# Performance work log

Measured on AMD Instinct MI355X. Metric: run time of the kernel, lower is better.

## Reference

```python
import jax, jax.numpy as jnp
import numpy as np

B, SEQ, DIM, D, K = 32, 2048, 512, 512, 128


def _ln(x, g, b, eps=1e-5):
    m = x.mean(-1, keepdims=True)
    v = ((x - m) ** 2).mean(-1, keepdims=True)
    return (x - m) / jnp.sqrt(v + eps) * g + b


def _gelu(v):
    return jax.nn.gelu(v, approximate=False)


def _diff_topk(s, k, t):
    # s: (B, N) scores; iterative relaxed top-k (Xie & Ermon style).
    def step(carry, _):
        a = jax.nn.softmax(carry / t, axis=-1)
        carry = carry + jnp.log(jnp.clip(1.0 - a, 1e-6, 1.0))
        return carry, a
    _, Ws = jax.lax.scan(step, s, None, length=k)  # (k, B, N)
    return jnp.transpose(Ws, (1, 0, 2))            # (B, k, N)


def setup_inputs():
    key = jax.random.key(0)
    ks = jax.random.split(key, 6)
    w = lambda k_, shape: jax.random.normal(k_, shape, dtype=jnp.float32) * 0.02
    return {
        'x': jax.random.normal(ks[0], (B, SEQ, DIM), dtype=jnp.float32),
        'tau': jnp.array(0.0, dtype=jnp.float32),
        'ln1_g': jnp.ones((DIM,), jnp.float32), 'ln1_b': jnp.zeros((DIM,), jnp.float32),
        'W1': w(ks[1], (DIM, D)), 'b1': jnp.zeros((D,), jnp.float32),
        'ln2_g': jnp.ones((SEQ,), jnp.float32), 'ln2_b': jnp.zeros((SEQ,), jnp.float32),
        'W2': w(ks[2], (SEQ, SEQ)), 'b2': jnp.zeros((SEQ,), jnp.float32),
        'ln3_g': jnp.ones((D,), jnp.float32), 'ln3_b': jnp.zeros((D,), jnp.float32),
        'W3': w(ks[3], (D, D + 1)), 'b3': jnp.zeros((D + 1,), jnp.float32),
        'ln4_g': jnp.ones((D,), jnp.float32), 'ln4_b': jnp.zeros((D,), jnp.float32),
        'W4': w(ks[4], (D, DIM)), 'b4': jnp.zeros((DIM,), jnp.float32),
    }


def reference(x, tau, ln1_g, ln1_b, W1, b1, ln2_g, ln2_b, W2, b2,
              ln3_g, ln3_b, W3, b3, ln4_g, ln4_b, W4, b4):
    # tok_proj: LN(dim) -> Linear(dim, D) -> GELU
    x_tok = _gelu(_ln(x, ln1_g, ln1_b) @ W1 + b1)                  # (B, N, D)
    # ch_proj over the token axis: LN(seq) -> Linear(seq, seq) -> GELU
    xt = jnp.swapaxes(x_tok, 1, 2)                                  # (B, D, N)
    x_ch = jnp.swapaxes(_gelu(_ln(xt, ln2_g, ln2_b) @ W2 + b2), 1, 2)
    # proj -> split score | features
    h = _ln(x_tok + x_ch, ln3_g, ln3_b) @ W3 + b3                   # (B, N, D+1)
    x_score, x_proj = h[..., 0], h[..., 1:]
    t = jax.nn.sigmoid(jnp.clip(tau, -2.0, 5.0))
    Wmat = _diff_topk(x_score, K, t)                                # (B, k, N)
    Z = jnp.einsum('bkn,bnd->bkd', Wmat, x_proj)                    # soft gather
    Y = jnp.einsum('bkn,bkd->bnd', Wmat, Z)                         # soft scatter
    return _ln(x_proj + Y, ln4_g, ln4_b) @ W4 + b4                  # (B, N, dim)
```

## Files before the change

kernel.cpp:

```cpp
#include <hip/hip_runtime.h>
#include <math.h>

#define B_   32
#define SEQ_ 2048
#define DIM_ 512
#define KSEL 128

typedef _Float16 f16;
typedef _Float16 half8 __attribute__((ext_vector_type(8)));
typedef float floatx4 __attribute__((ext_vector_type(4)));

#define LSTRH 40

__device__ __forceinline__ float gelu_exact(float v) {
  return 0.5f * v * (1.0f + erff(v * 0.70710678118654752440f));
}

__global__ __launch_bounds__(256) void rowstats512(const float* __restrict__ X,
                                                   float* __restrict__ mean,
                                                   float* __restrict__ rstd) {
  int row = blockIdx.x * 4 + (threadIdx.x >> 6);
  int l = threadIdx.x & 63;
  const float4* p = (const float4*)(X + (size_t)row * 512);
  float4 v0 = p[l * 2], v1 = p[l * 2 + 1];
  float s = v0.x + v0.y + v0.z + v0.w + v1.x + v1.y + v1.z + v1.w;
  float q = v0.x*v0.x + v0.y*v0.y + v0.z*v0.z + v0.w*v0.w
          + v1.x*v1.x + v1.y*v1.y + v1.z*v1.z + v1.w*v1.w;
#pragma unroll
  for (int off = 32; off > 0; off >>= 1) {
    s += __shfl_down(s, off);
    q += __shfl_down(q, off);
  }
  if (l == 0) {
    float m = s * (1.0f / 512.0f);
    float var = q * (1.0f / 512.0f) - m * m;
    mean[row] = m;
    rstd[row] = rsqrtf(var + 1e-5f);
  }
}

__global__ __launch_bounds__(256) void rowstats512_f16(const f16* __restrict__ X,
                                                       float* __restrict__ mean,
                                                       float* __restrict__ rstd) {
  int row = blockIdx.x * 4 + (threadIdx.x >> 6);
  int l = threadIdx.x & 63;
  half8 h = *(const half8*)(X + (size_t)row * 512 + l * 8);
  float s = 0.f, q = 0.f;
#pragma unroll
  for (int i = 0; i < 8; ++i) { float v = (float)h[i]; s += v; q += v * v; }
#pragma unroll
  for (int off = 32; off > 0; off >>= 1) {
    s += __shfl_down(s, off);
    q += __shfl_down(q, off);
  }
  if (l == 0) {
    float m = s * (1.0f / 512.0f);
    float var = q * (1.0f / 512.0f) - m * m;
    mean[row] = m;
    rstd[row] = rsqrtf(var + 1e-5f);
  }
}

__global__ __launch_bounds__(512) void colstats_part(const f16* __restrict__ xtok,
                                                     float2* __restrict__ part) {
  int b = blockIdx.x >> 3, pr = blockIdx.x & 7;
  int d = threadIdx.x;
  const f16* src = xtok + ((size_t)b * SEQ_ + (size_t)pr * 256) * 512 + d;
  float s = 0.f, q = 0.f;
#pragma unroll 4
  for (int i = 0; i < 256; ++i) {
    float v = (float)src[(size_t)i * 512];
    s += v; q += v * v;
  }
  part[(size_t)blockIdx.x * 512 + d] = make_float2(s, q);
}

__global__ __launch_bounds__(256) void colstats_fin(const float2* __restrict__ part,
                                                    float* __restrict__ mean,
                                                    float* __restrict__ rstd) {
  int idx = blockIdx.x * 256 + threadIdx.x;
  int b = idx >> 9;
  float s = 0.f, q = 0.f;
#pragma unroll
  for (int p = 0; p < 8; ++p) {
    float2 v = part[((size_t)(b * 8 + p)) * 512 + (idx & 511)];
    s += v.x; q += v.y;
  }
  float m = s * (1.0f / 2048.0f);
  mean[idx] = m;
  rstd[idx] = rsqrtf(q * (1.0f / 2048.0f) - m * m + 1e-5f);
}

template <typename T>
__global__ __launch_bounds__(256) void transpose_cvt(const T* __restrict__ src,
                                                     f16* __restrict__ dst,
                                                     int R, int C, long sb, long db) {
  __shared__ float tile[32][33];
  const T* s = src + (long)blockIdx.z * sb;
  f16* d = dst + (long)blockIdx.z * db;
  int c0 = blockIdx.x * 32, r0 = blockIdx.y * 32;
  int tx = threadIdx.x, ty = threadIdx.y;
#pragma unroll
  for (int i = 0; i < 4; ++i) {
    int r = r0 + ty + i * 8, c = c0 + tx;
    if (r < R && c < C) tile[ty + i * 8][tx] = (float)s[(long)r * C + c];
  }
  __syncthreads();
#pragma unroll
  for (int i = 0; i < 4; ++i) {
    int c = c0 + ty + i * 8, r = r0 + tx;
    if (c < C && r < R) d[(long)c * R + r] = (f16)tile[tx][ty + i * 8];
  }
}

__global__ __launch_bounds__(256) void trans2_kernel(const f16* __restrict__ xtok,
    const float* __restrict__ mean2, const float* __restrict__ rstd2,
    const float* __restrict__ g2, const float* __restrict__ bl2,
    f16* __restrict__ A2) {
  __shared__ float tile[32][33];
  int b = blockIdx.z;
  const f16* src = xtok + (long)b * SEQ_ * 512;
  f16* dst = A2 + (long)b * 512 * SEQ_;
  int d0 = blockIdx.x * 32, s0 = blockIdx.y * 32;
  int tx = threadIdx.x, ty = threadIdx.y;
  float m = mean2[b * 512 + d0 + tx];
  float rs = rstd2[b * 512 + d0 + tx];
#pragma unroll
  for (int i = 0; i < 4; ++i) {
    int s = s0 + ty + i * 8;
    float v = (float)src[(long)s * 512 + d0 + tx];
    tile[ty + i * 8][tx] = (v - m) * rs * g2[s] + bl2[s];
  }
  __syncthreads();
#pragma unroll
  for (int i = 0; i < 4; ++i) {
    int d = d0 + ty + i * 8, s = s0 + tx;
    dst[(long)d * SEQ_ + s] = (f16)tile[tx][ty + i * 8];
  }
}


__device__ __forceinline__ void stage_f16(const f16* __restrict__ src, long ld,
                                          int row0, int k0, f16* S, int t) {
  int row = t >> 1, kc = (t & 1) * 16;
  const f16* p = src + (long)(row0 + row) * ld + k0 + kc;
  half8 v0 = *(const half8*)(p);
  half8 v1 = *(const half8*)(p + 8);
  *(half8*)(S + row * LSTRH + kc) = v0;
  *(half8*)(S + row * LSTRH + kc + 8) = v1;
}

__device__ __forceinline__ void stage_a_f32(const float* __restrict__ src, long ld,
                                            int row0, int k0, f16* S, int t) {
  int row = t >> 1, kc = (t & 1) * 16;
  const float* p = src + (long)(row0 + row) * ld + k0 + kc;
  float v[16];
#pragma unroll
  for (int i = 0; i < 4; ++i) {
    float4 q = ((const float4*)p)[i];
    v[i * 4 + 0] = q.x; v[i * 4 + 1] = q.y; v[i * 4 + 2] = q.z; v[i * 4 + 3] = q.w;
  }
  half8 o0, o1;
#pragma unroll
  for (int i = 0; i < 8; ++i) { o0[i] = (f16)v[i]; o1[i] = (f16)v[i + 8]; }
  *(half8*)(S + row * LSTRH + kc) = o0;
  *(half8*)(S + row * LSTRH + kc + 8) = o1;
}

__device__ __forceinline__ void stage_a_ln_f32(const float* __restrict__ src, long ld,
    const float* __restrict__ mean, const float* __restrict__ rstd,
    const float* __restrict__ g, const float* __restrict__ bl,
    int row0, int k0, f16* S, int t) {
  int row = t >> 1, kc = (t & 1) * 16;
  int r = row0 + row, c = k0 + kc;
  float m = mean[r], sd = rstd[r];
  const float* p = src + (long)r * ld + c;
  float v[16], gv[16], bv[16];
#pragma unroll
  for (int i = 0; i < 4; ++i) {
    float4 q = ((const float4*)p)[i];
    v[i*4+0]=q.x; v[i*4+1]=q.y; v[i*4+2]=q.z; v[i*4+3]=q.w;
    float4 gq = ((const float4*)(g + c))[i];
    gv[i*4+0]=gq.x; gv[i*4+1]=gq.y; gv[i*4+2]=gq.z; gv[i*4+3]=gq.w;
    float4 bq = ((const float4*)(bl + c))[i];
    bv[i*4+0]=bq.x; bv[i*4+1]=bq.y; bv[i*4+2]=bq.z; bv[i*4+3]=bq.w;
  }
  half8 o0, o1;
#pragma unroll
  for (int i = 0; i < 8; ++i) {
    o0[i] = (f16)((v[i] - m) * sd * gv[i] + bv[i]);
    o1[i] = (f16)((v[i + 8] - m) * sd * gv[i + 8] + bv[i + 8]);
  }
  *(half8*)(S + row * LSTRH + kc) = o0;
  *(half8*)(S + row * LSTRH + kc + 8) = o1;
}

__device__ __forceinline__ void stage_a_ln_f16(const f16* __restrict__ src, long ld,
    const float* __restrict__ mean, const float* __restrict__ rstd,
    const float* __restrict__ g, const float* __restrict__ bl,
    int row0, int k0, f16* S, int t) {
  int row = t >> 1, kc = (t & 1) * 16;
  int r = row0 + row, c = k0 + kc;
  float m = mean[r], sd = rstd[r];
  const f16* p = src + (long)r * ld + c;
  half8 h0 = *(const half8*)(p);
  half8 h1 = *(const half8*)(p + 8);
  float gv[16], bv[16];
#pragma unroll
  for (int i = 0; i < 4; ++i) {
    float4 gq = ((const float4*)(g + c))[i];
    gv[i*4+0]=gq.x; gv[i*4+1]=gq.y; gv[i*4+2]=gq.z; gv[i*4+3]=gq.w;
    float4 bq = ((const float4*)(bl + c))[i];
    bv[i*4+0]=bq.x; bv[i*4+1]=bq.y; bv[i*4+2]=bq.z; bv[i*4+3]=bq.w;
  }
  half8 o0, o1;
#pragma unroll
  for (int i = 0; i < 8; ++i) {
    o0[i] = (f16)(((float)h0[i] - m) * sd * gv[i] + bv[i]);
    o1[i] = (f16)(((float)h1[i] - m) * sd * gv[i + 8] + bv[i + 8]);
  }
  *(half8*)(S + row * LSTRH + kc) = o0;
  *(half8*)(S + row * LSTRH + kc + 8) = o1;
}

__device__ __forceinline__ void mfma_step(const f16* As, const f16* Bs, int lane,
                                          int wr, int wc, floatx4 acc[4][4]) {
  int kc = (lane >> 4) * 8;
  int rl = lane & 15;
  half8 a[4], b[4];
#pragma unroll
  for (int mi = 0; mi < 4; ++mi)
    a[mi] = *(const half8*)(As + (wr * 64 + mi * 16 + rl) * LSTRH + kc);
#pragma unroll
  for (int ni = 0; ni < 4; ++ni)
    b[ni] = *(const half8*)(Bs + (wc * 64 + ni * 16 + rl) * LSTRH + kc);
#pragma unroll
  for (int mi = 0; mi < 4; ++mi)
#pragma unroll
    for (int ni = 0; ni < 4; ++ni)
      acc[mi][ni] = __builtin_amdgcn_mfma_f32_16x16x32_f16(a[mi], b[ni], acc[mi][ni], 0, 0, 0);
}

#define GEMM_PROLOG \
  __shared__ f16 As[128 * LSTRH]; \
  __shared__ f16 Bs[128 * LSTRH]; \
  int t = threadIdx.x; \
  int lane = t & 63, w = t >> 6, wr = w >> 1, wc = w & 1; \
  floatx4 acc[4][4]; \
  _Pragma("unroll") for (int mi = 0; mi < 4; ++mi) \
  _Pragma("unroll") for (int ni = 0; ni < 4; ++ni) acc[mi][ni] = (floatx4){0.f,0.f,0.f,0.f};

__global__ __launch_bounds__(256) void g1_kernel(const float* __restrict__ x,
    const float* __restrict__ mean, const float* __restrict__ rstd,
    const float* __restrict__ g1, const float* __restrict__ bl1,
    const f16* __restrict__ W1T, const float* __restrict__ b1,
    f16* __restrict__ xtok) {
  GEMM_PROLOG
  int m0 = blockIdx.y * 128, n0 = blockIdx.x * 128;
  for (int k0 = 0; k0 < 512; k0 += 32) {
    stage_a_ln_f32(x, 512, mean, rstd, g1, bl1, m0, k0, As, t);
    stage_f16(W1T, 512, n0, k0, Bs, t);
    __syncthreads();
    mfma_step(As, Bs, lane, wr, wc, acc);
    __syncthreads();
  }
#pragma unroll
  for (int mi = 0; mi < 4; ++mi)
#pragma unroll
    for (int ni = 0; ni < 4; ++ni) {
      int c = n0 + wc * 64 + ni * 16 + (lane & 15);
      float bias = b1[c];
      int r0 = m0 + wr * 64 + mi * 16 + (lane >> 4) * 4;
#pragma unroll
      for (int j = 0; j < 4; ++j)
        xtok[(long)(r0 + j) * 512 + c] = (f16)gelu_exact(acc[mi][ni][j] + bias);
    }
}

__global__ __launch_bounds__(256) void g2_kernel(const f16* __restrict__ W2T,
    const f16* __restrict__ A2, const float* __restrict__ b2,
    const f16* __restrict__ xtok, f16* __restrict__ xsum) {
  GEMM_PROLOG
  int b = blockIdx.z;
  int m0 = blockIdx.y * 128, n0 = blockIdx.x * 128;
  const f16* A2b = A2 + (long)b * 512 * SEQ_;
  const f16* xtb = xtok + (long)b * SEQ_ * 512;
  f16* xsb = xsum + (long)b * SEQ_ * 512;
  for (int k0 = 0; k0 < SEQ_; k0 += 32) {
    stage_f16(W2T, SEQ_, m0, k0, As, t);
    stage_f16(A2b, SEQ_, n0, k0, Bs, t);
    __syncthreads();
    mfma_step(As, Bs, lane, wr, wc, acc);
    __syncthreads();
  }
#pragma unroll
  for (int mi = 0; mi < 4; ++mi)
#pragma unroll
    for (int ni = 0; ni < 4; ++ni) {
      int c = n0 + wc * 64 + ni * 16 + (lane & 15);
      int r0 = m0 + wr * 64 + mi * 16 + (lane >> 4) * 4;
#pragma unroll
      for (int j = 0; j < 4; ++j) {
        int r = r0 + j;
        long idx = (long)r * 512 + c;
        float v = gelu_exact(acc[mi][ni][j] + b2[r]);
        xsb[idx] = (f16)((float)xtb[idx] + v);
      }
    }
}

__global__ __launch_bounds__(256) void g3_kernel(const f16* __restrict__ xsum,
    const float* __restrict__ mean, const float* __restrict__ rstd,
    const float* __restrict__ g3, const float* __restrict__ bl3,
    const f16* __restrict__ BT , const float* __restrict__ b3,
    f16* __restrict__ xproj) {
  GEMM_PROLOG
  int m0 = blockIdx.y * 128, n0 = blockIdx.x * 128;
  for (int k0 = 0; k0 < 512; k0 += 32) {
    stage_a_ln_f16(xsum, 512, mean, rstd, g3, bl3, m0, k0, As, t);
    stage_f16(BT, 512, n0, k0, Bs, t);
    __syncthreads();
    mfma_step(As, Bs, lane, wr, wc, acc);
    __syncthreads();
  }
#pragma unroll
  for (int mi = 0; mi < 4; ++mi)
#pragma unroll
    for (int ni = 0; ni < 4; ++ni) {
      int c = n0 + wc * 64 + ni * 16 + (lane & 15);
      float bias = b3[c + 1];
      int r0 = m0 + wr * 64 + mi * 16 + (lane >> 4) * 4;
#pragma unroll
      for (int j = 0; j < 4; ++j)
        xproj[(long)(r0 + j) * 512 + c] = (f16)(acc[mi][ni][j] + bias);
    }
}

__global__ __launch_bounds__(256) void score_kernel(const f16* __restrict__ xsum,
    const float* __restrict__ mean, const float* __restrict__ rstd,
    const float* __restrict__ g3, const float* __restrict__ bl3,
    const f16* __restrict__ w3c , const float* __restrict__ b3,
    float* __restrict__ xscore) {
  int row = blockIdx.x * 4 + (threadIdx.x >> 6);
  int l = threadIdx.x & 63;
  float m = mean[row], sd = rstd[row];
  half8 h = *(const half8*)(xsum + (long)row * 512 + l * 8);
  half8 wv = *(const half8*)(w3c + l * 8);
  float acc = 0.f;
#pragma unroll
  for (int i = 0; i < 8; ++i) {
    int d = l * 8 + i;
    float v = ((float)h[i] - m) * sd * g3[d] + bl3[d];
    acc += v * (float)wv[i];
  }
#pragma unroll
  for (int off = 32; off > 0; off >>= 1) acc += __shfl_down(acc, off);
  if (l == 0) xscore[row] = acc + b3[0];
}

__global__ __launch_bounds__(256) void topk_kernel(const float* __restrict__ xscore,
                                                   const float* __restrict__ tau,
                                                   float* __restrict__ Wm) {
  int b = blockIdx.x, t = threadIdx.x;
  __shared__ float red[4];
  float tv = fminf(fmaxf(tau[0], -2.0f), 5.0f);
  float temp = 1.0f / (1.0f + expf(-tv));
  float it = 1.0f / temp;
  float c[8];
  const float* xs = xscore + (size_t)b * SEQ_;
#pragma unroll
  for (int i = 0; i < 8; ++i) c[i] = xs[t * 8 + i];
  for (int k = 0; k < KSEL; ++k) {
    float e[8];
    float p = 0.f;
#pragma unroll
    for (int i = 0; i < 8; ++i) { e[i] = expf(c[i] * it); p += e[i]; }
#pragma unroll
    for (int off = 32; off > 0; off >>= 1) p += __shfl_down(p, off);
    if ((t & 63) == 0) red[t >> 6] = p;
    __syncthreads();
    float S = red[0] + red[1] + red[2] + red[3];
    float iS = 1.0f / S;
    float a[8];
#pragma unroll
    for (int i = 0; i < 8; ++i) a[i] = e[i] * iS;
    float* dst = Wm + ((size_t)b * KSEL + k) * SEQ_ + t * 8;
    *(float4*)(dst) = make_float4(a[0], a[1], a[2], a[3]);
    *(float4*)(dst + 4) = make_float4(a[4], a[5], a[6], a[7]);
#pragma unroll
    for (int i = 0; i < 8; ++i) c[i] += logf(fmaxf(1.0f - a[i], 1e-6f));
    __syncthreads();
  }
}

__global__ __launch_bounds__(256) void gz_kernel(const float* __restrict__ Wm,
    const f16* __restrict__ xprojT, float* __restrict__ Z) {
  GEMM_PROLOG
  int b = blockIdx.z;
  int n0 = blockIdx.x * 128;
  const float* A = Wm + (long)b * KSEL * SEQ_;
  const f16* BT = xprojT + (long)b * 512 * SEQ_;
  float* Zb = Z + (long)b * KSEL * 512;
  for (int k0 = 0; k0 < SEQ_; k0 += 32) {
    stage_a_f32(A, SEQ_, 0, k0, As, t);
    stage_f16(BT, SEQ_, n0, k0, Bs, t);
    __syncthreads();
    mfma_step(As, Bs, lane, wr, wc, acc);
    __syncthreads();
  }
#pragma unroll
  for (int mi = 0; mi < 4; ++mi)
#pragma unroll
    for (int ni = 0; ni < 4; ++ni) {
      int c = n0 + wc * 64 + ni * 16 + (lane & 15);
      int r0 = wr * 64 + mi * 16 + (lane >> 4) * 4;
#pragma unroll
      for (int j = 0; j < 4; ++j)
        Zb[(long)(r0 + j) * 512 + c] = acc[mi][ni][j];
    }
}

__global__ __launch_bounds__(256) void gy_kernel(const f16* __restrict__ WmT,
    const f16* __restrict__ ZT, const f16* __restrict__ xproj,
    f16* __restrict__ rbuf) {
  GEMM_PROLOG
  int b = blockIdx.z;
  int m0 = blockIdx.y * 128, n0 = blockIdx.x * 128;
  const f16* A = WmT + (long)b * SEQ_ * KSEL;
  const f16* BT = ZT + (long)b * 512 * KSEL;
  const f16* xpb = xproj + (long)b * SEQ_ * 512;
  f16* rb = rbuf + (long)b * SEQ_ * 512;
  for (int k0 = 0; k0 < KSEL; k0 += 32) {
    stage_f16(A, KSEL, m0, k0, As, t);
    stage_f16(BT, KSEL, n0, k0, Bs, t);
    __syncthreads();
    mfma_step(As, Bs, lane, wr, wc, acc);
    __syncthreads();
  }
#pragma unroll
  for (int mi = 0; mi < 4; ++mi)
#pragma unroll
    for (int ni = 0; ni < 4; ++ni) {
      int c = n0 + wc * 64 + ni * 16 + (lane & 15);
      int r0 = m0 + wr * 64 + mi * 16 + (lane >> 4) * 4;
#pragma unroll
      for (int j = 0; j < 4; ++j) {
        long idx = (long)(r0 + j) * 512 + c;
        rb[idx] = (f16)((float)xpb[idx] + acc[mi][ni][j]);
      }
    }
}

__global__ __launch_bounds__(256) void g4_kernel(const f16* __restrict__ rbuf,
    const float* __restrict__ mean, const float* __restrict__ rstd,
    const float* __restrict__ g4, const float* __restrict__ bl4,
    const f16* __restrict__ W4T, const float* __restrict__ b4,
    float* __restrict__ out) {
  GEMM_PROLOG
  int m0 = blockIdx.y * 128, n0 = blockIdx.x * 128;
  for (int k0 = 0; k0 < 512; k0 += 32) {
    stage_a_ln_f16(rbuf, 512, mean, rstd, g4, bl4, m0, k0, As, t);
    stage_f16(W4T, 512, n0, k0, Bs, t);
    __syncthreads();
    mfma_step(As, Bs, lane, wr, wc, acc);
    __syncthreads();
  }
#pragma unroll
  for (int mi = 0; mi < 4; ++mi)
#pragma unroll
    for (int ni = 0; ni < 4; ++ni) {
      int c = n0 + wc * 64 + ni * 16 + (lane & 15);
      float bias = b4[c];
      int r0 = m0 + wr * 64 + mi * 16 + (lane >> 4) * 4;
#pragma unroll
      for (int j = 0; j < 4; ++j)
        out[(long)(r0 + j) * 512 + c] = acc[mi][ni][j] + bias;
    }
}

extern "C" void kernel_launch(void* const* d_in, const int* in_sizes, int n_in,
                              void* d_out, int out_size, void* d_ws, size_t ws_size,
                              hipStream_t stream) {
  const float* x    = (const float*)d_in[0];
  const float* tau  = (const float*)d_in[1];
  const float* g1   = (const float*)d_in[2];
  const float* bl1  = (const float*)d_in[3];
  const float* W1   = (const float*)d_in[4];
  const float* b1   = (const float*)d_in[5];
  const float* g2   = (const float*)d_in[6];
  const float* bl2  = (const float*)d_in[7];
  const float* W2   = (const float*)d_in[8];
  const float* b2   = (const float*)d_in[9];
  const float* g3   = (const float*)d_in[10];
  const float* bl3  = (const float*)d_in[11];
  const float* W3   = (const float*)d_in[12];
  const float* b3   = (const float*)d_in[13];
  const float* g4   = (const float*)d_in[14];
  const float* bl4  = (const float*)d_in[15];
  const float* W4   = (const float*)d_in[16];
  const float* b4   = (const float*)d_in[17];
  float* out = (float*)d_out;

  const long NTOK = (long)B_ * SEQ_;

  char* ws = (char*)d_ws;
  f16* regA   = (f16*)(ws);
  f16* regB   = (f16*)(ws + (64l << 20));
  float* Z    = (float*)(ws + (128l << 20));
  f16* ZT     = (f16*)(ws + (136l << 20));
  f16* WmT    = (f16*)(ws + (140l << 20));
  f16* W1T    = (f16*)(ws + (156l << 20));
  f16* W2T    = (f16*)(ws + (157l << 20));
  f16* W3T    = (f16*)(ws + (165l << 20));
  f16* W4T    = (f16*)(ws + (166l << 20));
  float* xscore = (float*)(ws + (167l << 20));
  float* meanA  = (float*)(ws + (168l << 20));
  float* rstdA  = meanA + NTOK;
  float* mean2  = rstdA + NTOK;
  float* rstd2  = mean2 + B_ * 512;
  float2* part  = (float2*)(rstd2 + B_ * 512);

  f16* xtok   = (f16*)d_out;
  float* Wm   = (float*)((char*)d_out + (64l << 20));
  f16* xprojT = (f16*)d_out;

  f16* A2    = regA;
  f16* xsum  = regB;
  f16* xproj = regA;
  f16* rbuf  = regB;

  dim3 tb(32, 8);

  transpose_cvt<float><<<dim3(16, 16, 1), tb, 0, stream>>>(W1, W1T, 512, 512, 0, 0);
  transpose_cvt<float><<<dim3(64, 64, 1), tb, 0, stream>>>(W2, W2T, 2048, 2048, 0, 0);
  transpose_cvt<float><<<dim3(17, 16, 1), tb, 0, stream>>>(W3, W3T, 512, 513, 0, 0);
  transpose_cvt<float><<<dim3(16, 16, 1), tb, 0, stream>>>(W4, W4T, 512, 512, 0, 0);

  rowstats512<<<NTOK / 4, 256, 0, stream>>>(x, meanA, rstdA);
  g1_kernel<<<dim3(4, 512), 256, 0, stream>>>(x, meanA, rstdA, g1, bl1, W1T, b1, xtok);

  colstats_part<<<B_ * 8, 512, 0, stream>>>(xtok, part);
  colstats_fin<<<64, 256, 0, stream>>>(part, mean2, rstd2);
  trans2_kernel<<<dim3(16, 64, B_), tb, 0, stream>>>(xtok, mean2, rstd2, g2, bl2, A2);
  g2_kernel<<<dim3(4, 16, B_), 256, 0, stream>>>(W2T, A2, b2, xtok, xsum);

  rowstats512_f16<<<NTOK / 4, 256, 0, stream>>>(xsum, meanA, rstdA);
  score_kernel<<<NTOK / 4, 256, 0, stream>>>(xsum, meanA, rstdA, g3, bl3, W3T, b3, xscore);
  g3_kernel<<<dim3(4, 512), 256, 0, stream>>>(xsum, meanA, rstdA, g3, bl3, W3T + 512, b3, xproj);

  topk_kernel<<<B_, 256, 0, stream>>>(xscore, tau, Wm);

  transpose_cvt<f16><<<dim3(16, 64, B_), tb, 0, stream>>>(xproj, xprojT, 2048, 512,
      (long)SEQ_ * 512, (long)512 * SEQ_);
  transpose_cvt<float><<<dim3(64, 4, B_), tb, 0, stream>>>(Wm, WmT, 128, 2048,
      (long)KSEL * SEQ_, (long)SEQ_ * KSEL);

  gz_kernel<<<dim3(4, 1, B_), 256, 0, stream>>>(Wm, xprojT, Z);
  transpose_cvt<float><<<dim3(16, 4, B_), tb, 0, stream>>>(Z, ZT, 128, 512,
      (long)KSEL * 512, (long)512 * KSEL);

  gy_kernel<<<dim3(4, 16, B_), 256, 0, stream>>>(WmT, ZT, xproj, rbuf);

  rowstats512_f16<<<NTOK / 4, 256, 0, stream>>>(rbuf, meanA, rstdA);
  g4_kernel<<<dim3(4, 512), 256, 0, stream>>>(rbuf, meanA, rstdA, g4, bl4, W4T, b4, out);
}
```

Baseline: 980.8 us.

## Stage f16 GEMM tiles via global_load_lds and split-K the gather GEMM

```diff
diff --git a/kernel.cpp b/kernel.cpp
--- a/kernel.cpp
+++ b/kernel.cpp
@@ -10,7 +10,7 @@
 typedef _Float16 half8 __attribute__((ext_vector_type(8)));
 typedef float floatx4 __attribute__((ext_vector_type(4)));
 
-#define LSTRH 40
+#define LSTR2 32
 
 __device__ __forceinline__ float gelu_exact(float v) {
   return 0.5f * v * (1.0f + erff(v * 0.70710678118654752440f));
@@ -140,31 +140,19 @@
 }
 
 
-__device__ __forceinline__ void stage_f16(const f16* __restrict__ src, long ld,
+__device__ __forceinline__ void stage_gll(const f16* __restrict__ src, long ld,
                                           int row0, int k0, f16* S, int t) {
-  int row = t >> 1, kc = (t & 1) * 16;
-  const f16* p = src + (long)(row0 + row) * ld + k0 + kc;
-  half8 v0 = *(const half8*)(p);
-  half8 v1 = *(const half8*)(p + 8);
-  *(half8*)(S + row * LSTRH + kc) = v0;
-  *(half8*)(S + row * LSTRH + kc + 8) = v1;
-}
-
-__device__ __forceinline__ void stage_a_f32(const float* __restrict__ src, long ld,
-                                            int row0, int k0, f16* S, int t) {
-  int row = t >> 1, kc = (t & 1) * 16;
-  const float* p = src + (long)(row0 + row) * ld + k0 + kc;
-  float v[16];
-#pragma unroll
-  for (int i = 0; i < 4; ++i) {
-    float4 q = ((const float4*)p)[i];
-    v[i * 4 + 0] = q.x; v[i * 4 + 1] = q.y; v[i * 4 + 2] = q.z; v[i * 4 + 3] = q.w;
-  }
-  half8 o0, o1;
-#pragma unroll
-  for (int i = 0; i < 8; ++i) { o0[i] = (f16)v[i]; o1[i] = (f16)v[i + 8]; }
-  *(half8*)(S + row * LSTRH + kc) = o0;
-  *(half8*)(S + row * LSTRH + kc + 8) = o1;
+  int w = t >> 6, lane = t & 63;
+  int r = lane >> 2, c8 = (lane & 3) * 8;
+#pragma unroll
+  for (int i = 0; i < 2; ++i) {
+    int chunk = w * 2 + i;
+    const f16* g = src + (long)(row0 + chunk * 16 + r) * ld + k0 + c8;
+    f16* l = S + chunk * 16 * LSTR2;
+    __builtin_amdgcn_global_load_lds(
+        (const __attribute__((address_space(1))) void*)g,
+        (__attribute__((address_space(3))) void*)l, 16, 0, 0);
+  }
 }
 
 __device__ __forceinline__ void stage_a_ln_f32(const float* __restrict__ src, long ld,
@@ -191,8 +179,8 @@
     o0[i] = (f16)((v[i] - m) * sd * gv[i] + bv[i]);
     o1[i] = (f16)((v[i + 8] - m) * sd * gv[i + 8] + bv[i + 8]);
   }
-  *(half8*)(S + row * LSTRH + kc) = o0;
-  *(half8*)(S + row * LSTRH + kc + 8) = o1;
+  *(half8*)(S + row * LSTR2 + kc) = o0;
+  *(half8*)(S + row * LSTR2 + kc + 8) = o1;
 }
 
 __device__ __forceinline__ void stage_a_ln_f16(const f16* __restrict__ src, long ld,
@@ -219,8 +207,8 @@
     o0[i] = (f16)(((float)h0[i] - m) * sd * gv[i] + bv[i]);
     o1[i] = (f16)(((float)h1[i] - m) * sd * gv[i + 8] + bv[i + 8]);
   }
-  *(half8*)(S + row * LSTRH + kc) = o0;
-  *(half8*)(S + row * LSTRH + kc + 8) = o1;
+  *(half8*)(S + row * LSTR2 + kc) = o0;
+  *(half8*)(S + row * LSTR2 + kc + 8) = o1;
 }
 
 __device__ __forceinline__ void mfma_step(const f16* As, const f16* Bs, int lane,
@@ -230,10 +218,10 @@
   half8 a[4], b[4];
 #pragma unroll
   for (int mi = 0; mi < 4; ++mi)
-    a[mi] = *(const half8*)(As + (wr * 64 + mi * 16 + rl) * LSTRH + kc);
+    a[mi] = *(const half8*)(As + (wr * 64 + mi * 16 + rl) * LSTR2 + kc);
 #pragma unroll
   for (int ni = 0; ni < 4; ++ni)
-    b[ni] = *(const half8*)(Bs + (wc * 64 + ni * 16 + rl) * LSTRH + kc);
+    b[ni] = *(const half8*)(Bs + (wc * 64 + ni * 16 + rl) * LSTR2 + kc);
 #pragma unroll
   for (int mi = 0; mi < 4; ++mi)
 #pragma unroll
@@ -242,8 +230,8 @@
 }
 
 #define GEMM_PROLOG \
-  __shared__ f16 As[128 * LSTRH]; \
-  __shared__ f16 Bs[128 * LSTRH]; \
+  __shared__ __attribute__((aligned(16))) f16 As[128 * LSTR2]; \
+  __shared__ __attribute__((aligned(16))) f16 Bs[128 * LSTR2]; \
   int t = threadIdx.x; \
   int lane = t & 63, w = t >> 6, wr = w >> 1, wc = w & 1; \
   floatx4 acc[4][4]; \
@@ -259,7 +247,7 @@
   int m0 = blockIdx.y * 128, n0 = blockIdx.x * 128;
   for (int k0 = 0; k0 < 512; k0 += 32) {
     stage_a_ln_f32(x, 512, mean, rstd, g1, bl1, m0, k0, As, t);
-    stage_f16(W1T, 512, n0, k0, Bs, t);
+    stage_gll(W1T, 512, n0, k0, Bs, t);
     __syncthreads();
     mfma_step(As, Bs, lane, wr, wc, acc);
     __syncthreads();
@@ -287,8 +275,8 @@
   const f16* xtb = xtok + (long)b * SEQ_ * 512;
   f16* xsb = xsum + (long)b * SEQ_ * 512;
   for (int k0 = 0; k0 < SEQ_; k0 += 32) {
-    stage_f16(W2T, SEQ_, m0, k0, As, t);
-    stage_f16(A2b, SEQ_, n0, k0, Bs, t);
+    stage_gll(W2T, SEQ_, m0, k0, As, t);
+    stage_gll(A2b, SEQ_, n0, k0, Bs, t);
     __syncthreads();
     mfma_step(As, Bs, lane, wr, wc, acc);
     __syncthreads();
@@ -318,7 +306,7 @@
   int m0 = blockIdx.y * 128, n0 = blockIdx.x * 128;
   for (int k0 = 0; k0 < 512; k0 += 32) {
     stage_a_ln_f16(xsum, 512, mean, rstd, g3, bl3, m0, k0, As, t);
-    stage_f16(BT, 512, n0, k0, Bs, t);
+    stage_gll(BT, 512, n0, k0, Bs, t);
     __syncthreads();
     mfma_step(As, Bs, lane, wr, wc, acc);
     __syncthreads();
@@ -360,7 +348,7 @@
 
 __global__ __launch_bounds__(256) void topk_kernel(const float* __restrict__ xscore,
                                                    const float* __restrict__ tau,
-                                                   float* __restrict__ Wm) {
+                                                   f16* __restrict__ Wm) {
   int b = blockIdx.x, t = threadIdx.x;
   __shared__ float red[4];
   float tv = fminf(fmaxf(tau[0], -2.0f), 5.0f);
@@ -382,28 +370,28 @@
     float S = red[0] + red[1] + red[2] + red[3];
     float iS = 1.0f / S;
     float a[8];
-#pragma unroll
-    for (int i = 0; i < 8; ++i) a[i] = e[i] * iS;
-    float* dst = Wm + ((size_t)b * KSEL + k) * SEQ_ + t * 8;
-    *(float4*)(dst) = make_float4(a[0], a[1], a[2], a[3]);
-    *(float4*)(dst + 4) = make_float4(a[4], a[5], a[6], a[7]);
+    half8 h;
+#pragma unroll
+    for (int i = 0; i < 8; ++i) { a[i] = e[i] * iS; h[i] = (f16)a[i]; }
+    *(half8*)(Wm + ((size_t)b * KSEL + k) * SEQ_ + t * 8) = h;
 #pragma unroll
     for (int i = 0; i < 8; ++i) c[i] += logf(fmaxf(1.0f - a[i], 1e-6f));
     __syncthreads();
   }
 }
 
-__global__ __launch_bounds__(256) void gz_kernel(const float* __restrict__ Wm,
-    const f16* __restrict__ xprojT, float* __restrict__ Z) {
+__global__ __launch_bounds__(256) void gz_kernel(const f16* __restrict__ Wm,
+    const f16* __restrict__ xprojT, float* __restrict__ Zpart) {
   GEMM_PROLOG
-  int b = blockIdx.z;
+  int b = blockIdx.z, kc = blockIdx.y;
   int n0 = blockIdx.x * 128;
-  const float* A = Wm + (long)b * KSEL * SEQ_;
+  const f16* A = Wm + (long)b * KSEL * SEQ_;
   const f16* BT = xprojT + (long)b * 512 * SEQ_;
-  float* Zb = Z + (long)b * KSEL * 512;
-  for (int k0 = 0; k0 < SEQ_; k0 += 32) {
-    stage_a_f32(A, SEQ_, 0, k0, As, t);
-    stage_f16(BT, SEQ_, n0, k0, Bs, t);
+  float* Zb = Zpart + ((long)b * 2 + kc) * KSEL * 512;
+  int kbeg = kc * 1024, kend = kbeg + 1024;
+  for (int k0 = kbeg; k0 < kend; k0 += 32) {
+    stage_gll(A, SEQ_, 0, k0, As, t);
+    stage_gll(BT, SEQ_, n0, k0, Bs, t);
     __syncthreads();
     mfma_step(As, Bs, lane, wr, wc, acc);
     __syncthreads();
@@ -418,6 +406,28 @@
       for (int j = 0; j < 4; ++j)
         Zb[(long)(r0 + j) * 512 + c] = acc[mi][ni][j];
     }
+}
+
+__global__ __launch_bounds__(256) void ztrans_kernel(const float* __restrict__ Zpart,
+                                                     f16* __restrict__ ZT) {
+  __shared__ float tile[32][33];
+  int b = blockIdx.z;
+  int c0 = blockIdx.x * 32, r0 = blockIdx.y * 32;
+  int tx = threadIdx.x, ty = threadIdx.y;
+  const float* p0 = Zpart + ((long)b * 2 + 0) * KSEL * 512;
+  const float* p1 = Zpart + ((long)b * 2 + 1) * KSEL * 512;
+#pragma unroll
+  for (int i = 0; i < 4; ++i) {
+    int r = r0 + ty + i * 8, c = c0 + tx;
+    tile[ty + i * 8][tx] = p0[(long)r * 512 + c] + p1[(long)r * 512 + c];
+  }
+  __syncthreads();
+  f16* d = ZT + (long)b * 512 * KSEL;
+#pragma unroll
+  for (int i = 0; i < 4; ++i) {
+    int c = c0 + ty + i * 8, r = r0 + tx;
+    d[(long)c * KSEL + r] = (f16)tile[tx][ty + i * 8];
+  }
 }
 
 __global__ __launch_bounds__(256) void gy_kernel(const f16* __restrict__ WmT,
@@ -431,8 +441,8 @@
   const f16* xpb = xproj + (long)b * SEQ_ * 512;
   f16* rb = rbuf + (long)b * SEQ_ * 512;
   for (int k0 = 0; k0 < KSEL; k0 += 32) {
-    stage_f16(A, KSEL, m0, k0, As, t);
-    stage_f16(BT, KSEL, n0, k0, Bs, t);
+    stage_gll(A, KSEL, m0, k0, As, t);
+    stage_gll(BT, KSEL, n0, k0, Bs, t);
     __syncthreads();
     mfma_step(As, Bs, lane, wr, wc, acc);
     __syncthreads();
@@ -460,7 +470,7 @@
   int m0 = blockIdx.y * 128, n0 = blockIdx.x * 128;
   for (int k0 = 0; k0 < 512; k0 += 32) {
     stage_a_ln_f16(rbuf, 512, mean, rstd, g4, bl4, m0, k0, As, t);
-    stage_f16(W4T, 512, n0, k0, Bs, t);
+    stage_gll(W4T, 512, n0, k0, Bs, t);
     __syncthreads();
     mfma_step(As, Bs, lane, wr, wc, acc);
     __syncthreads();
@@ -506,23 +516,23 @@
   char* ws = (char*)d_ws;
   f16* regA   = (f16*)(ws);
   f16* regB   = (f16*)(ws + (64l << 20));
-  float* Z    = (float*)(ws + (128l << 20));
-  f16* ZT     = (f16*)(ws + (136l << 20));
-  f16* WmT    = (f16*)(ws + (140l << 20));
-  f16* W1T    = (f16*)(ws + (156l << 20));
-  f16* W2T    = (f16*)(ws + (157l << 20));
-  f16* W3T    = (f16*)(ws + (165l << 20));
-  f16* W4T    = (f16*)(ws + (166l << 20));
-  float* xscore = (float*)(ws + (167l << 20));
-  float* meanA  = (float*)(ws + (168l << 20));
+  float* Zpart = (float*)(ws + (128l << 20));
+  f16* W2T    = (f16*)(ws + (144l << 20));
+  f16* W1T    = (f16*)(ws + (152l << 20));
+  f16* W3T    = (f16*)(ws + (153l << 20));
+  f16* W4T    = (f16*)(ws + (154l << 20));
+  float* xscore = (float*)(ws + (155l << 20));
+  float* meanA  = (float*)(ws + (156l << 20));
   float* rstdA  = meanA + NTOK;
   float* mean2  = rstdA + NTOK;
   float* rstd2  = mean2 + B_ * 512;
   float2* part  = (float2*)(rstd2 + B_ * 512);
 
   f16* xtok   = (f16*)d_out;
-  float* Wm   = (float*)((char*)d_out + (64l << 20));
   f16* xprojT = (f16*)d_out;
+  f16* Wm     = (f16*)((char*)d_out + (64l << 20));
+  f16* WmT    = (f16*)((char*)d_out + (80l << 20));
+  f16* ZT     = (f16*)((char*)d_out + (96l << 20));
 
   f16* A2    = regA;
   f16* xsum  = regB;
@@ -552,12 +562,11 @@
 
   transpose_cvt<f16><<<dim3(16, 64, B_), tb, 0, stream>>>(xproj, xprojT, 2048, 512,
       (long)SEQ_ * 512, (long)512 * SEQ_);
-  transpose_cvt<float><<<dim3(64, 4, B_), tb, 0, stream>>>(Wm, WmT, 128, 2048,
+  transpose_cvt<f16><<<dim3(64, 4, B_), tb, 0, stream>>>(Wm, WmT, 128, 2048,
       (long)KSEL * SEQ_, (long)SEQ_ * KSEL);
 
-  gz_kernel<<<dim3(4, 1, B_), 256, 0, stream>>>(Wm, xprojT, Z);
-  transpose_cvt<float><<<dim3(16, 4, B_), tb, 0, stream>>>(Z, ZT, 128, 512,
-      (long)KSEL * 512, (long)512 * KSEL);
+  gz_kernel<<<dim3(4, 2, B_), 256, 0, stream>>>(Wm, xprojT, Zpart);
+  ztrans_kernel<<<dim3(16, 4, B_), tb, 0, stream>>>(Zpart, ZT);
 
   gy_kernel<<<dim3(4, 16, B_), 256, 0, stream>>>(WmT, ZT, xproj, rbuf);
 
```

Result: faster. 878.3 us (-10.4%).
